# Kernel optimization log

Measured on AMD Instinct MI355X. Metric: run time of the kernel, lower is better.

The kernel has to match this reference:

```python
import jax, jax.numpy as jnp
import numpy as np

B, FIN, V, X, Y, Z = 2, 32, 768, 8, 8, 8
K, FOUT = 5, 32
NNZ = V * 8  # ~8 neighbors per vertex


def setup_inputs() -> dict:
    key = jax.random.key(0)
    k1, k2, k3, k4, k5 = jax.random.split(key, 5)
    std = np.sqrt(2.0 / (FIN * K)).astype(np.float32)
    return {
        "lap_rows": jax.random.randint(k1, (NNZ,), 0, V, dtype=jnp.int32),
        "lap_cols": jax.random.randint(k2, (NNZ,), 0, V, dtype=jnp.int32),
        "lap_vals": jax.random.normal(k3, (NNZ,), dtype=jnp.float32) * 0.1,
        "x": jax.random.normal(k4, (B, FIN, V, X, Y, Z), dtype=jnp.float32),
        "weight": jax.random.normal(k5, (K, FIN, FOUT), dtype=jnp.float32) * std,
        "bias": jnp.full((FOUT,), 0.01, dtype=jnp.float32),
    }


def reference(lap_rows, lap_cols, lap_vals, x, weight, bias):
    Bb, Fin, Vv, Xx, Yy, Zz = x.shape
    Kk, _, Fout = weight.shape

    def spmm(v):  # sparse [V,V] @ dense [V,D]
        return jax.ops.segment_sum(lap_vals[:, None] * v[lap_cols],
                                   lap_rows, num_segments=Vv)

    # [B,Fin,V,X,Y,Z] -> [V, Fin*B*X*Y*Z]
    x0 = jnp.transpose(x, (2, 1, 0, 3, 4, 5)).reshape(Vv, -1)
    xs = [x0]
    if Kk > 1:
        x1 = spmm(x0)
        xs.append(x1)
        for _ in range(2, Kk):
            x2 = 2.0 * spmm(x1) - x0
            xs.append(x2)
            x0, x1 = x1, x2
    basis = jnp.stack(xs, axis=0)  # [K, V, Fin*B*X*Y*Z]
    basis = basis.reshape(Kk, Vv, Fin, Bb, Xx, Yy, Zz)
    basis = jnp.transpose(basis, (3, 1, 4, 5, 6, 0, 2))  # [B,V,X,Y,Z,K,Fin]
    out = basis.reshape(-1, Kk * Fin) @ weight.reshape(Kk * Fin, Fout)
    out = out.reshape(Bb, Vv, Xx, Yy, Zz, Fout)
    out = jnp.transpose(out, (0, 5, 1, 2, 3, 4))  # [B,Fout,V,X,Y,Z]
    return out + bias[None, :, None, None, None, None]
```

## Files before the change

kernel.cpp:

```cpp
#include <hip/hip_runtime.h>
#include <stdint.h>

#define V      768
#define FINC   32
#define FOUTC  32
#define XYZ    512
#define NB     2
#define ROWP   40
#define MAXDEG 32
#define EROWS  36

typedef unsigned short u16;
typedef unsigned int   u32;
typedef short bf16x8 __attribute__((ext_vector_type(8)));
typedef float f32x4  __attribute__((ext_vector_type(4)));
typedef float f32x2  __attribute__((ext_vector_type(2)));

__device__ __forceinline__ u16 f2bf(float f) {
  u32 u = __float_as_uint(f);
  u32 r = u + 0x7fffu + ((u >> 16) & 1u);
  return (u16)(r >> 16);
}
__device__ __forceinline__ float bflo(u32 w) { return __uint_as_float(w << 16); }
__device__ __forceinline__ float bfhi(u32 w) { return __uint_as_float(w & 0xffff0000u); }
__device__ __forceinline__ float bfhi_raw(u32 w) { return __uint_as_float(w); }
__device__ __forceinline__ u32 cvtpk_bf16(float lo, float hi) {
  u32 r;
  asm("v_cvt_pk_bf16_f32 %0, %1, %2" : "=v"(r) : "v"(lo), "v"(hi));
  return r;
}

__global__ __launch_bounds__(64) void build_ell(const int* __restrict__ rows,
                                                const int* __restrict__ cols,
                                                const float* __restrict__ vals,
                                                int nnz,
                                                int2* __restrict__ epair,
                                                int* __restrict__ deg) {
  int v = blockIdx.x;
  int lane = threadIdx.x;
  int cnt = 0;
  for (int base = 0; base < nnz; base += 64) {
    int i = base + lane;
    bool m = (i < nnz) && (rows[i] == v);
    unsigned long long mask = __ballot(m);
    if (m) {
      int pos = cnt + __popcll(mask & ((1ull << lane) - 1ull));
      if (pos < MAXDEG)
        epair[v * MAXDEG + pos] = make_int2(cols[i], __float_as_int(vals[i]));
    }
    cnt += __popcll(mask);
  }
  int d = cnt < MAXDEG ? cnt : MAXDEG;
  for (int p = d + lane; p < MAXDEG; p += 64)
    epair[v * MAXDEG + p] = make_int2(0, 0);
  if (lane == 0) deg[v] = d;
}

__global__ __launch_bounds__(V) void sort_rows(const int2* __restrict__ epair,
                                               const int* __restrict__ deg,
                                               int2* __restrict__ ep3,
                                               int* __restrict__ perm,
                                               int* __restrict__ inv_g,
                                               int* __restrict__ wtrip) {
  __shared__ int sdeg[V];
  __shared__ u16 sinv[V];
  int v = threadIdx.x;
  int d = deg[v];
  sdeg[v] = d;
  __syncthreads();
  int r = 0;
  for (int u = 0; u < V; ++u) {
    int du = sdeg[u];
    r += (du > d) || (du == d && u < v);
  }
  const unsigned long long GPK = 0x8495A6B73210ull;
  int w = (int)((GPK >> (4 * (r >> 6))) & 15ull);
  int p = w * 64 + (r & 63);
  perm[p] = v;
  inv_g[v] = p;
  sinv[v] = (u16)p;
  if ((r & 63) == 0) wtrip[w] = d;
  __syncthreads();
  for (int e = 0; e < EROWS; ++e) {
    int2 o = make_int2(0, 0);
    if (e < d) {
      int2 pe = epair[v * MAXDEG + e];
      o = make_int2((int)sinv[pe.x] * (ROWP * 2), pe.y);
    }
    ep3[e * V + p] = o;
  }
}

#define TXV 12
__global__ __launch_bounds__(512) void transpose_x(const float* __restrict__ x,
                                                   const int* __restrict__ perm,
                                                   u16* __restrict__ xT) {
  __shared__ u16 TL[384][66];
  __shared__ int PV[TXV];
  int g = blockIdx.x;
  int b = g >> 9, pvt = (g >> 3) & 63, xt = g & 7;
  int pv0 = pvt * TXV;
  int xyz0 = xt * 64;
  int t = threadIdx.x;
  if (t < TXV) PV[t] = perm[pv0 + t];
  __syncthreads();
  int lane = t & 63, pg = t >> 6;
#pragma unroll
  for (int st = 0; st < 48; ++st) {
    int pair = st * 8 + pg;
    int vloc = pair >> 5, f = pair & 31;
    float val = x[((size_t)(b * FINC + f) * V + PV[vloc]) * XYZ + xyz0 + lane];
    TL[pair][lane] = f2bf(val);
  }
  __syncthreads();
  int s = t & 7, xyz = t >> 3;
  u32* dst = (u32*)(xT + ((size_t)(b * XYZ + xyz0 + xyz) * V + pv0) * FINC);
#pragma unroll
  for (int it = 0; it < 24; ++it) {
    int i = s + 8 * it;
    u32 lo = TL[2 * i][xyz], hi = TL[2 * i + 1][xyz];
    dst[i] = lo | (hi << 16);
  }
}

__global__ __launch_bounds__(1024, 4) void cheb_main(
    const u16* __restrict__ xT, const int2* __restrict__ ep3,
    const int* __restrict__ perm, const int* __restrict__ wtrip,
    const float* __restrict__ weight, const float* __restrict__ bias,
    u32* __restrict__ stage) {
  __shared__ __align__(16) u16   CUR[V * ROWP];
  __shared__ __align__(16) u16   PRV[V * ROWP];
  __shared__ __align__(16) uint4 WF[5][2][64];
  __shared__ u16 PRM[V];
  __shared__ int WT[12];

  int g = blockIdx.x;
  int xcd = g & 7;
  int u = g >> 3;
  int phase = u >> 5;
  int xyz = xcd * 32 + (u & 31) + (phase & 1) * 256;
  int b = phase >> 1;
  int slice = b * XYZ + xyz;

  int tid = threadIdx.x;
  int lane = tid & 63;
  int w = tid >> 6;
  int l15 = lane & 15, l4 = lane >> 4;
  bool gath = tid < V;

  if (tid < 640) {
    int k = tid >> 7, n = (tid >> 6) & 1, ln = tid & 63;
    int a15 = ln & 15, a4 = ln >> 4;
    u32 pw[4];
#pragma unroll
    for (int p = 0; p < 4; ++p) {
      float w0 = weight[(size_t)(k * FINC + a4 * 8 + 2 * p) * FOUTC + n * 16 + a15];
      float w1 = weight[(size_t)(k * FINC + a4 * 8 + 2 * p + 1) * FOUTC + n * 16 + a15];
      pw[p] = (u32)f2bf(w0) | ((u32)f2bf(w1) << 16);
    }
    WF[k][n][ln] = make_uint4(pw[0], pw[1], pw[2], pw[3]);
  }
  if (tid < 12) WT[tid] = wtrip[tid];
  if (gath) PRM[tid] = (u16)perm[tid];
  float bsv[2] = {bias[l15], bias[16 + l15]};

  if (gath) {
    const uint4* src = (const uint4*)(xT + (size_t)slice * V * FINC) + tid * 4;
    uint4* dst = (uint4*)(CUR + tid * ROWP);
#pragma unroll
    for (int j = 0; j < 4; ++j) dst[j] = src[j];
  }
  __syncthreads();

  int trip = 0;
  if (w < 12) trip = __builtin_amdgcn_readfirstlane(WT[w]);
  const int2* pp = ep3 + tid;

  f32x4 acc[3][2];
#pragma unroll
  for (int a = 0; a < 3; ++a)
#pragma unroll
    for (int n = 0; n < 2; ++n) acc[a][n] = (f32x4){0.f, 0.f, 0.f, 0.f};

  auto gemm_acc = [&](int k) {
    bf16x8 bn0 = *(const bf16x8*)&WF[k][0][lane];
    bf16x8 bn1 = *(const bf16x8*)&WF[k][1][lane];
#pragma unroll
    for (int a = 0; a < 3; ++a) {
      int row = w * 48 + a * 16 + l15;
      bf16x8 af = *(const bf16x8*)(CUR + row * ROWP + l4 * 8);
      acc[a][0] = __builtin_amdgcn_mfma_f32_16x16x32_bf16(af, bn0, acc[a][0], 0, 0, 0);
      acc[a][1] = __builtin_amdgcn_mfma_f32_16x16x32_bf16(af, bn1, acc[a][1], 0, 0, 0);
    }
  };

  f32x2 fa2[16];
  auto fma_edge = [&](float fv, uint4 qa, uint4 qb, uint4 qc, uint4 qd) {
    f32x2 fv2 = {fv, fv};
    u32 wq[16] = {qa.x, qa.y, qa.z, qa.w, qb.x, qb.y, qb.z, qb.w,
                  qc.x, qc.y, qc.z, qc.w, qd.x, qd.y, qd.z, qd.w};
#pragma unroll
    for (int p = 0; p < 16; ++p) {
      f32x2 s = {bflo(wq[p]), bfhi_raw(wq[p])};
      fa2[p] += fv2 * s;
    }
  };
  auto gather = [&]() {
#pragma unroll
    for (int j = 0; j < 16; ++j) fa2[j] = (f32x2){0.f, 0.f};
    int trips = (trip + 1) & ~1;
    int2 r0 = pp[0], r1 = pp[V], r2 = pp[2 * V];
    const uint4* s0 = (const uint4*)((const char*)CUR + (u32)r0.x);
    uint4 A0 = s0[0], A1 = s0[1], A2 = s0[2], A3 = s0[3];
    for (int e = 0; e < trips; e += 2) {
      const uint4* s1 = (const uint4*)((const char*)CUR + (u32)r1.x);
      uint4 B0 = s1[0], B1 = s1[1], B2 = s1[2], B3 = s1[3];
      int2 n3 = pp[(e + 3) * V];
      fma_edge(__int_as_float(r0.y), A0, A1, A2, A3);
      const uint4* s2 = (const uint4*)((const char*)CUR + (u32)r2.x);
      A0 = s2[0]; A1 = s2[1]; A2 = s2[2]; A3 = s2[3];
      int2 n4 = pp[(e + 4) * V];
      fma_edge(__int_as_float(r1.y), B0, B1, B2, B3);
      r0 = r2; r1 = n3; r2 = n4;
    }
  };

  auto do_update = [&](bool first) {
    uint4* cp = (uint4*)(CUR + tid * ROWP);
    uint4* qp = (uint4*)(PRV + tid * ROWP);
    uint4 c[4];
#pragma unroll
    for (int j = 0; j < 4; ++j) c[j] = cp[j];
    u32 npk[16];
    if (first) {
#pragma unroll
      for (int j = 0; j < 16; ++j) npk[j] = cvtpk_bf16(fa2[j][0], fa2[j][1]);
    } else {
      uint4 pv[4];
#pragma unroll
      for (int j = 0; j < 4; ++j) pv[j] = qp[j];
      u32 wp[16] = {pv[0].x, pv[0].y, pv[0].z, pv[0].w, pv[1].x, pv[1].y, pv[1].z, pv[1].w,
                    pv[2].x, pv[2].y, pv[2].z, pv[2].w, pv[3].x, pv[3].y, pv[3].z, pv[3].w};
#pragma unroll
      for (int j = 0; j < 16; ++j) {
        float t0 = 2.f * fa2[j][0] - bflo(wp[j]);
        float t1 = 2.f * fa2[j][1] - bfhi(wp[j]);
        npk[j] = cvtpk_bf16(t0, t1);
      }
    }
#pragma unroll
    for (int j = 0; j < 4; ++j) {
      qp[j] = c[j];
      cp[j] = make_uint4(npk[4 * j], npk[4 * j + 1], npk[4 * j + 2], npk[4 * j + 3]);
    }
  };

#pragma unroll
  for (int ph = 0; ph <= 3; ++ph) {
    gemm_acc(ph);
    if (gath) gather();
    __syncthreads();
    if (gath) do_update(ph == 0);
    __syncthreads();
  }

  gemm_acc(4);

  u32* stg = stage + (size_t)slice * (V * 16);
#pragma unroll
  for (int a = 0; a < 3; ++a) {
#pragma unroll
    for (int r = 0; r < 4; ++r) {
      int vr = PRM[w * 48 + a * 16 + l4 * 4 + r];
      u32 pk = cvtpk_bf16(acc[a][0][r] + bsv[0], acc[a][1][r] + bsv[1]);
      stg[vr * 16 + l15] = pk;
    }
  }
}

#define TO_VT  12
#define TO_PAD 193
__global__ __launch_bounds__(512) void transpose_out(const u32* __restrict__ stage,
                                                     float* __restrict__ out) {
  __shared__ u32 T[64 * TO_PAD];
  int g = blockIdx.x;
  int b = g >> 9, vt = (g >> 3) & 63, xt = g & 7;
  int v0 = vt * TO_VT;
  int xyz0 = xt * 64;
  int t = threadIdx.x;
  const u32* base = stage + (size_t)(b * XYZ + xyz0) * (V * 16) + v0 * 16;
#pragma unroll
  for (int i = 0; i < 6; ++i) {
    int idx4 = i * 512 + t;
    int j = idx4 / 48;
    int c4 = idx4 - j * 48;
    uint4 q = *(const uint4*)(base + (size_t)j * (V * 16) + c4 * 4);
    int w0 = c4 * 4;
    T[j * TO_PAD + w0]     = q.x;
    T[j * TO_PAD + w0 + 1] = q.y;
    T[j * TO_PAD + w0 + 2] = q.z;
    T[j * TO_PAD + w0 + 3] = q.w;
  }
  __syncthreads();
  int wv = t >> 6, lane = t & 63;
#pragma unroll
  for (int i = 0; i < 48; ++i) {
    int fout = wv * 4 + i / 12;
    int vv = i % 12;
    u32 pk = T[lane * TO_PAD + vv * 16 + (fout & 15)];
    float val = (fout < 16) ? bflo(pk) : bfhi(pk);
    out[((size_t)(b * FOUTC + fout) * V + v0 + vv) * XYZ + xyz0 + lane] = val;
  }
}

extern "C" void kernel_launch(void* const* d_in, const int* in_sizes, int n_in,
                              void* d_out, int out_size, void* d_ws, size_t ws_size,
                              hipStream_t stream) {
  const int*   lap_rows = (const int*)d_in[0];
  const int*   lap_cols = (const int*)d_in[1];
  const float* lap_vals = (const float*)d_in[2];
  const float* x        = (const float*)d_in[3];
  const float* weight   = (const float*)d_in[4];
  const float* bias     = (const float*)d_in[5];
  float* out = (float*)d_out;
  int nnz = in_sizes[0];

  char* ws = (char*)d_ws;
  const size_t XT_BYTES = (size_t)NB * XYZ * V * FINC * sizeof(u16);
  const size_t EP_BYTES = (size_t)V * MAXDEG * 8;
  const size_t E3_BYTES = (size_t)EROWS * V * 8;
  u16*  xT    = (u16*)ws;
  u32*  stg   = (u32*)ws;
  int2* epair = (int2*)(ws + XT_BYTES);
  int2* ep3   = (int2*)(ws + XT_BYTES + EP_BYTES);
  int*  deg   = (int*)(ws + XT_BYTES + EP_BYTES + E3_BYTES);
  int*  perm  = (int*)(ws + XT_BYTES + EP_BYTES + E3_BYTES + 3072);
  int*  inv_g = (int*)(ws + XT_BYTES + EP_BYTES + E3_BYTES + 6144);
  int*  wtrip = (int*)(ws + XT_BYTES + EP_BYTES + E3_BYTES + 9216);

  hipLaunchKernelGGL(build_ell, dim3(V), dim3(64), 0, stream,
                     lap_rows, lap_cols, lap_vals, nnz, epair, deg);
  hipLaunchKernelGGL(sort_rows, dim3(1), dim3(V), 0, stream,
                     epair, deg, ep3, perm, inv_g, wtrip);
  hipLaunchKernelGGL(transpose_x, dim3(NB * 64 * 8), dim3(512), 0, stream,
                     x, perm, xT);
  hipLaunchKernelGGL(cheb_main, dim3(NB * XYZ), dim3(1024), 0, stream,
                     xT, ep3, perm, wtrip, weight, bias, stg);
  hipLaunchKernelGGL(transpose_out, dim3(NB * 64 * 8), dim3(512), 0, stream,
                     stg, out);
}
```

Before: 204.6 us.

## Vectorize transpose loads/stores and split gather into two half-row passes

The input transpose now loads float4 from x, packs to bf16 with v_cvt_pk, and stores uint2 into a padded u32 LDS tile. The output transpose writes float2 instead of scalar floats. In the main kernel the SpMM gather is split into two half-row passes with a 4-deep edge pipeline, which halves the live accumulator registers and deepens memory-level parallelism. EROWS is raised to 40 so the edge table is padded for the longer prefetch. The trade-off is that the second half-row pass reads the edge indices a second time, and the first half is held as bf16 in pk0 before the update. That half is therefore rounded to bf16 before the 2x-minus-previous update, which adds an extra rounding step.

```diff
diff --git a/kernel.cpp b/kernel.cpp
--- a/kernel.cpp
+++ b/kernel.cpp
@@ -8,7 +8,7 @@
 #define NB     2
 #define ROWP   40
 #define MAXDEG 32
-#define EROWS  36
+#define EROWS  40
 
 typedef unsigned short u16;
 typedef unsigned int   u32;
@@ -95,7 +95,7 @@
 __global__ __launch_bounds__(512) void transpose_x(const float* __restrict__ x,
                                                    const int* __restrict__ perm,
                                                    u16* __restrict__ xT) {
-  __shared__ u16 TL[384][66];
+  __shared__ u32 TL2[384 * 34];
   __shared__ int PV[TXV];
   int g = blockIdx.x;
   int b = g >> 9, pvt = (g >> 3) & 63, xt = g & 7;
@@ -104,21 +104,26 @@
   int t = threadIdx.x;
   if (t < TXV) PV[t] = perm[pv0 + t];
   __syncthreads();
-  int lane = t & 63, pg = t >> 6;
-#pragma unroll
-  for (int st = 0; st < 48; ++st) {
-    int pair = st * 8 + pg;
-    int vloc = pair >> 5, f = pair & 31;
-    float val = x[((size_t)(b * FINC + f) * V + PV[vloc]) * XYZ + xyz0 + lane];
-    TL[pair][lane] = f2bf(val);
-  }
-  __syncthreads();
+  int q = t & 15;
+  int rgrp = t >> 4;
+#pragma unroll
+  for (int st = 0; st < 12; ++st) {
+    int row = st * 32 + rgrp;
+    int vloc = row >> 5, f = row & 31;
+    const float4 xv = *(const float4*)&x[((size_t)(b * FINC + f) * V + PV[vloc]) * XYZ + xyz0 + 4 * q];
+    u32 A = cvtpk_bf16(xv.x, xv.y);
+    u32 B = cvtpk_bf16(xv.z, xv.w);
+    *(uint2*)&TL2[row * 34 + 2 * q] = make_uint2(A, B);
+  }
+  __syncthreads();
+  const u16* TL16 = (const u16*)TL2;
   int s = t & 7, xyz = t >> 3;
   u32* dst = (u32*)(xT + ((size_t)(b * XYZ + xyz0 + xyz) * V + pv0) * FINC);
 #pragma unroll
   for (int it = 0; it < 24; ++it) {
     int i = s + 8 * it;
-    u32 lo = TL[2 * i][xyz], hi = TL[2 * i + 1][xyz];
+    u32 lo = TL16[(2 * i) * 68 + xyz];
+    u32 hi = TL16[(2 * i + 1) * 68 + xyz];
     dst[i] = lo | (hi << 16);
   }
 }
@@ -194,71 +199,92 @@
     }
   };
 
-  f32x2 fa2[16];
-  auto fma_edge = [&](float fv, uint4 qa, uint4 qb, uint4 qc, uint4 qd) {
+  f32x2 fa[8];
+  auto fma_half = [&](float fv, uint4 qa, uint4 qb) {
     f32x2 fv2 = {fv, fv};
-    u32 wq[16] = {qa.x, qa.y, qa.z, qa.w, qb.x, qb.y, qb.z, qb.w,
-                  qc.x, qc.y, qc.z, qc.w, qd.x, qd.y, qd.z, qd.w};
-#pragma unroll
-    for (int p = 0; p < 16; ++p) {
+    u32 wq[8] = {qa.x, qa.y, qa.z, qa.w, qb.x, qb.y, qb.z, qb.w};
+#pragma unroll
+    for (int p = 0; p < 8; ++p) {
       f32x2 s = {bflo(wq[p]), bfhi_raw(wq[p])};
-      fa2[p] += fv2 * s;
+      fa[p] += fv2 * s;
     }
   };
-  auto gather = [&]() {
-#pragma unroll
-    for (int j = 0; j < 16; ++j) fa2[j] = (f32x2){0.f, 0.f};
-    int trips = (trip + 1) & ~1;
-    int2 r0 = pp[0], r1 = pp[V], r2 = pp[2 * V];
-    const uint4* s0 = (const uint4*)((const char*)CUR + (u32)r0.x);
-    uint4 A0 = s0[0], A1 = s0[1], A2 = s0[2], A3 = s0[3];
-    for (int e = 0; e < trips; e += 2) {
-      const uint4* s1 = (const uint4*)((const char*)CUR + (u32)r1.x);
-      uint4 B0 = s1[0], B1 = s1[1], B2 = s1[2], B3 = s1[3];
-      int2 n3 = pp[(e + 3) * V];
-      fma_edge(__int_as_float(r0.y), A0, A1, A2, A3);
-      const uint4* s2 = (const uint4*)((const char*)CUR + (u32)r2.x);
-      A0 = s2[0]; A1 = s2[1]; A2 = s2[2]; A3 = s2[3];
-      int2 n4 = pp[(e + 4) * V];
-      fma_edge(__int_as_float(r1.y), B0, B1, B2, B3);
-      r0 = r2; r1 = n3; r2 = n4;
+  auto gather_half = [&](int h) {
+#pragma unroll
+    for (int j = 0; j < 8; ++j) fa[j] = (f32x2){0.f, 0.f};
+    const char* base = (const char*)CUR + h * 32;
+    int2 p0 = pp[0], p1 = pp[V], p2 = pp[2 * V], p3 = pp[3 * V];
+    int2 a4 = pp[4 * V], a5 = pp[5 * V], a6 = pp[6 * V], a7 = pp[7 * V];
+    const uint4* s;
+    s = (const uint4*)(base + (u32)p0.x); uint4 D0a = s[0], D0b = s[1];
+    s = (const uint4*)(base + (u32)p1.x); uint4 D1a = s[0], D1b = s[1];
+    s = (const uint4*)(base + (u32)p2.x); uint4 D2a = s[0], D2b = s[1];
+    s = (const uint4*)(base + (u32)p3.x); uint4 D3a = s[0], D3b = s[1];
+    float v0 = __int_as_float(p0.y), v1 = __int_as_float(p1.y);
+    float v2 = __int_as_float(p2.y), v3 = __int_as_float(p3.y);
+    int tr = (trip + 3) & ~3;
+    for (int e = 0; e < tr; e += 4) {
+      int2 n0 = pp[(e + 8) * V], n1 = pp[(e + 9) * V];
+      int2 n2 = pp[(e + 10) * V], n3 = pp[(e + 11) * V];
+      fma_half(v0, D0a, D0b);
+      s = (const uint4*)(base + (u32)a4.x); D0a = s[0]; D0b = s[1];
+      v0 = __int_as_float(a4.y); a4 = n0;
+      fma_half(v1, D1a, D1b);
+      s = (const uint4*)(base + (u32)a5.x); D1a = s[0]; D1b = s[1];
+      v1 = __int_as_float(a5.y); a5 = n1;
+      fma_half(v2, D2a, D2b);
+      s = (const uint4*)(base + (u32)a6.x); D2a = s[0]; D2b = s[1];
+      v2 = __int_as_float(a6.y); a6 = n2;
+      fma_half(v3, D3a, D3b);
+      s = (const uint4*)(base + (u32)a7.x); D3a = s[0]; D3b = s[1];
+      v3 = __int_as_float(a7.y); a7 = n3;
     }
   };
 
+  u32 pk0[8];
   auto do_update = [&](bool first) {
     uint4* cp = (uint4*)(CUR + tid * ROWP);
     uint4* qp = (uint4*)(PRV + tid * ROWP);
-    uint4 c[4];
-#pragma unroll
-    for (int j = 0; j < 4; ++j) c[j] = cp[j];
-    u32 npk[16];
+    uint4 c0 = cp[0], c1 = cp[1], c2 = cp[2], c3 = cp[3];
+    u32 n[16];
     if (first) {
 #pragma unroll
-      for (int j = 0; j < 16; ++j) npk[j] = cvtpk_bf16(fa2[j][0], fa2[j][1]);
+      for (int j = 0; j < 8; ++j) n[j] = pk0[j];
+#pragma unroll
+      for (int j = 0; j < 8; ++j) n[8 + j] = cvtpk_bf16(fa[j][0], fa[j][1]);
     } else {
-      uint4 pv[4];
-#pragma unroll
-      for (int j = 0; j < 4; ++j) pv[j] = qp[j];
-      u32 wp[16] = {pv[0].x, pv[0].y, pv[0].z, pv[0].w, pv[1].x, pv[1].y, pv[1].z, pv[1].w,
-                    pv[2].x, pv[2].y, pv[2].z, pv[2].w, pv[3].x, pv[3].y, pv[3].z, pv[3].w};
-#pragma unroll
-      for (int j = 0; j < 16; ++j) {
-        float t0 = 2.f * fa2[j][0] - bflo(wp[j]);
-        float t1 = 2.f * fa2[j][1] - bfhi(wp[j]);
-        npk[j] = cvtpk_bf16(t0, t1);
+      uint4 q0 = qp[0], q1 = qp[1], q2 = qp[2], q3 = qp[3];
+      u32 wp[16] = {q0.x, q0.y, q0.z, q0.w, q1.x, q1.y, q1.z, q1.w,
+                    q2.x, q2.y, q2.z, q2.w, q3.x, q3.y, q3.z, q3.w};
+#pragma unroll
+      for (int j = 0; j < 8; ++j) {
+        float lo = 2.f * bflo(pk0[j]) - bflo(wp[j]);
+        float hi = 2.f * bfhi(pk0[j]) - bfhi(wp[j]);
+        n[j] = cvtpk_bf16(lo, hi);
       }
-    }
-#pragma unroll
-    for (int j = 0; j < 4; ++j) {
-      qp[j] = c[j];
-      cp[j] = make_uint4(npk[4 * j], npk[4 * j + 1], npk[4 * j + 2], npk[4 * j + 3]);
-    }
+#pragma unroll
+      for (int j = 0; j < 8; ++j) {
+        float lo = 2.f * fa[j][0] - bflo(wp[8 + j]);
+        float hi = 2.f * fa[j][1] - bfhi(wp[8 + j]);
+        n[8 + j] = cvtpk_bf16(lo, hi);
+      }
+    }
+    qp[0] = c0; qp[1] = c1; qp[2] = c2; qp[3] = c3;
+    cp[0] = make_uint4(n[0], n[1], n[2], n[3]);
+    cp[1] = make_uint4(n[4], n[5], n[6], n[7]);
+    cp[2] = make_uint4(n[8], n[9], n[10], n[11]);
+    cp[3] = make_uint4(n[12], n[13], n[14], n[15]);
   };
 
 #pragma unroll
   for (int ph = 0; ph <= 3; ++ph) {
     gemm_acc(ph);
-    if (gath) gather();
+    if (gath) {
+      gather_half(0);
+#pragma unroll
+      for (int j = 0; j < 8; ++j) pk0[j] = cvtpk_bf16(fa[j][0], fa[j][1]);
+      gather_half(1);
+    }
     __syncthreads();
     if (gath) do_update(ph == 0);
     __syncthreads();
@@ -302,14 +328,19 @@
     T[j * TO_PAD + w0 + 3] = q.w;
   }
   __syncthreads();
-  int wv = t >> 6, lane = t & 63;
-#pragma unroll
-  for (int i = 0; i < 48; ++i) {
-    int fout = wv * 4 + i / 12;
-    int vv = i % 12;
-    u32 pk = T[lane * TO_PAD + vv * 16 + (fout & 15)];
-    float val = (fout < 16) ? bflo(pk) : bfhi(pk);
-    out[((size_t)(b * FOUTC + fout) * V + v0 + vv) * XYZ + xyz0 + lane] = val;
+  int xyz2 = t & 31;
+  int grp = t >> 5;
+#pragma unroll
+  for (int i = 0; i < 24; ++i) {
+    int fout = grp * 2 + (i & 1);
+    int vv = i >> 1;
+    int col = vv * 16 + (fout & 15);
+    u32 pka = T[(2 * xyz2) * TO_PAD + col];
+    u32 pkb = T[(2 * xyz2 + 1) * TO_PAD + col];
+    float va = (fout < 16) ? bflo(pka) : bfhi(pka);
+    float vb = (fout < 16) ? bflo(pkb) : bfhi(pkb);
+    *(float2*)&out[((size_t)(b * FOUTC + fout) * V + v0 + vv) * XYZ + xyz0 + 2 * xyz2] =
+        make_float2(va, vb);
   }
 }
 
```

Result: slower. 214.1 us (+4.6%).
